# Optimization experiments

Measured on AMD Instinct MI355X. Metric: run time of the kernel, lower is better.

Reference implementation:

```python
import jax, jax.numpy as jnp
import numpy as np

L, U, D_IN, D_OUT, B = 6, 256, 784, 10, 32768  # num_layers, units, input_dim, output_dim, batch


def setup_inputs() -> dict:
    key = jax.random.key(0)
    ks = jax.random.split(key, 7)
    s = jnp.float32(0.05)  # keras 'random_normal' initializer stddev
    return {
        "x": jax.random.normal(ks[0], (B, D_IN), jnp.float32),
        "W_in": jax.random.normal(ks[1], (D_IN, U), jnp.float32) * s,
        "b_in": jax.random.normal(ks[2], (U,), jnp.float32) * s,
        "B0": jax.random.normal(ks[3], (L, U, U), jnp.float32) * s,   # per-layer B0
        "q": jax.random.normal(ks[4], (L, U), jnp.float32) * s,       # per-layer q
        "W_out": jax.random.normal(ks[5], (U, D_OUT), jnp.float32) * s,
        "b_out": jax.random.normal(ks[6], (D_OUT,), jnp.float32) * s,
    }


def reference(x, W_in, b_in, B0, q, W_out, b_out):
    u = W_in.shape[1]
    v0 = (x @ W_in + b_in).T          # (u, B)
    v1 = jnp.tanh(v0)                  # activation of layer 0 applied once before the loop

    def step(carry, params):
        v0, v1 = carry
        B0_l, q_l = params
        z = jnp.zeros((u, u), B0_l.dtype)
        # skew-symmetric block system [[0, B0], [-B0^T, 0]]
        A = jnp.block([[z, B0_l], [-B0_l.T, z]])           # (2u, 2u)
        rhs = jnp.concatenate([v0 + q_l[:, None], v1], 0)   # (2u, B)
        sol = jnp.linalg.solve(A, rhs)
        return (sol[:u], sol[u:]), None

    (v0, v1), _ = jax.lax.scan(step, (v0, v1), (B0, q))
    return v0.T @ W_out + b_out        # (B, D_OUT)
```

## Files before the change

kernel.cpp:

```cpp
#include <hip/hip_runtime.h>
#include <math.h>

#define NU      256
#define NLAYERS 6
#define NBATCH  32768
#define NDIN    784
#define NDOUT   10
#define NUSQ    65536

typedef unsigned short u16;
typedef __attribute__((ext_vector_type(8))) short s16x8;
typedef __attribute__((ext_vector_type(4))) float f32x4;

__device__ __forceinline__ u16 f2bf(float x) {
    union { float f; unsigned u; } a; a.f = x;
    const unsigned r = a.u + 0x7fffu + ((a.u >> 16) & 1u);
    return (u16)(r >> 16);
}
__device__ __forceinline__ float bf2f(u16 h) {
    union { unsigned u; float f; } a; a.u = ((unsigned)h) << 16; return a.f;
}

__device__ __forceinline__ void gl_lds16(const u16* g, u16* l) {
    __builtin_amdgcn_global_load_lds(
        (const __attribute__((address_space(1))) void*)g,
        (__attribute__((address_space(3))) void*)l, 16, 0, 0);
}

#define COL_CASES(BODY) \
    case 0:  BODY(0);  break; case 1:  BODY(1);  break; \
    case 2:  BODY(2);  break; case 3:  BODY(3);  break; \
    case 4:  BODY(4);  break; case 5:  BODY(5);  break; \
    case 6:  BODY(6);  break; case 7:  BODY(7);  break; \
    case 8:  BODY(8);  break; case 9:  BODY(9);  break; \
    case 10: BODY(10); break; case 11: BODY(11); break; \
    case 12: BODY(12); break; case 13: BODY(13); break; \
    case 14: BODY(14); break; case 15: BODY(15); break; \
    case 16: BODY(16); break; case 17: BODY(17); break; \
    case 18: BODY(18); break; case 19: BODY(19); break; \
    case 20: BODY(20); break; case 21: BODY(21); break; \
    case 22: BODY(22); break; case 23: BODY(23); break; \
    case 24: BODY(24); break; case 25: BODY(25); break; \
    case 26: BODY(26); break; case 27: BODY(27); break; \
    case 28: BODY(28); break; case 29: BODY(29); break; \
    case 30: BODY(30); break; case 31: BODY(31); break;

__global__ __launch_bounds__(512, 1) void fused_inv_ingemm(
    const float* __restrict__ B0, const float* __restrict__ qg,
    u16* __restrict__ wnnh, u16* __restrict__ wnnl,
    u16* __restrict__ wnth, u16* __restrict__ wntl,
    float* __restrict__ bq,
    const float* __restrict__ X, const float* __restrict__ Win,
    const float* __restrict__ bin,
    u16* __restrict__ V0h, u16* __restrict__ V0l,
    u16* __restrict__ V1h, u16* __restrict__ V1l)
{
    __shared__ __align__(16) float colv[2][256];
    __shared__ int   s_p[2];
    __shared__ float s_pv[2];
    __shared__ int   pivrow[256];
    __shared__ int   ilogrow[256];
    __shared__ float qs[256];
    __shared__ float part[8][256];
    __shared__ __align__(16) float As[16][128];
    __shared__ __align__(16) float Bs[16][128];

    const int tid = threadIdx.x;

    if (blockIdx.x < NLAYERS) {
        const int layer = blockIdx.x;
        const int ct = tid & 63;
        const int wv = tid >> 6;

        float a[32][4];
        const float* Ablk = B0 + (size_t)layer * NU * NU;
#pragma unroll
        for (int j = 0; j < 4; ++j) {
            const float* rp = Ablk + (size_t)(ct*4 + j)*NU + wv*32;
#pragma unroll
            for (int i = 0; i < 32; i += 4) {
                const float4 v = *(const float4*)(rp + i);
                a[i+0][j] = v.x; a[i+1][j] = v.y; a[i+2][j] = v.z; a[i+3][j] = v.w;
            }
        }

        int used = 0;

        for (int k = 0; k < 256; ++k) {
            const int wvk = k >> 5, ikk = k & 31, buf = k & 1;

            if (wv == wvk) {
                float c0, c1, c2, c3;
#define EXT(I) { c0 = a[I][0]; c1 = a[I][1]; c2 = a[I][2]; c3 = a[I][3]; }
                switch (ikk) { COL_CASES(EXT) }
#undef EXT
                float ba = -1.0f, bv = 1.0f; int br = 0;
                {
                    float av;
                    av = (used & 1) ? -1.0f : fabsf(c0);
                    if (av > ba) { ba = av; bv = c0; br = ct*4 + 0; }
                    av = (used & 2) ? -1.0f : fabsf(c1);
                    if (av > ba) { ba = av; bv = c1; br = ct*4 + 1; }
                    av = (used & 4) ? -1.0f : fabsf(c2);
                    if (av > ba) { ba = av; bv = c2; br = ct*4 + 2; }
                    av = (used & 8) ? -1.0f : fabsf(c3);
                    if (av > ba) { ba = av; bv = c3; br = ct*4 + 3; }
                }
#pragma unroll
                for (int off = 32; off > 0; off >>= 1) {
                    const float oa = __shfl_down(ba, off);
                    const float ov = __shfl_down(bv, off);
                    const int   orr = __shfl_down(br, off);
                    if (oa > ba) { ba = oa; bv = ov; br = orr; }
                }
                float4 cw; cw.x = c0; cw.y = c1; cw.z = c2; cw.w = c3;
                *(float4*)(&colv[buf][ct*4]) = cw;
                if (ct == 0) {
                    s_p[buf] = br;
                    s_pv[buf] = 1.0f / bv;
                    pivrow[k] = br;
                }
            }
            __syncthreads();

            const int   p      = __builtin_amdgcn_readfirstlane(s_p[buf]);
            const float pivinv = s_pv[buf];
            const int ctp = p >> 2, jp = p & 3;

            const float4 dv = *(const float4*)(&colv[buf][ct*4]);

            float t[32];
#define SEL(J) { _Pragma("unroll") for (int i = 0; i < 32; ++i) t[i] = a[i][J]; }
            switch (jp) {
                case 0: SEL(0) break; case 1: SEL(1) break;
                case 2: SEL(2) break; default: SEL(3) break;
            }
#undef SEL
            float prw[32];
#pragma unroll
            for (int i = 0; i < 32; ++i) prw[i] = __shfl(t[i], ctp) * pivinv;

            if (wv == wvk) {
#define ZCOL(I) { prw[I] = pivinv; a[I][0] = 0.0f; a[I][1] = 0.0f; a[I][2] = 0.0f; a[I][3] = 0.0f; }
                switch (ikk) { COL_CASES(ZCOL) }
#undef ZCOL
            }

            const float d0 = -dv.x, d1 = -dv.y, d2 = -dv.z, d3 = -dv.w;
#pragma unroll
            for (int i = 0; i < 32; ++i) {
                const float pw = prw[i];
                a[i][0] = fmaf(d0, pw, a[i][0]);
                a[i][1] = fmaf(d1, pw, a[i][1]);
                a[i][2] = fmaf(d2, pw, a[i][2]);
                a[i][3] = fmaf(d3, pw, a[i][3]);
            }

            const bool mine = (ct == ctp);
#define OWR(J) { _Pragma("unroll") for (int i = 0; i < 32; ++i) a[i][J] = mine ? prw[i] : a[i][J]; }
            switch (jp) {
                case 0: OWR(0) break; case 1: OWR(1) break;
                case 2: OWR(2) break; default: OWR(3) break;
            }
#undef OWR
            if (mine) used |= (1 << jp);
        }
        __syncthreads();

        if (tid < 256) { ilogrow[pivrow[tid]] = tid; qs[tid] = qg[(size_t)layer*NU + tid]; }
        __syncthreads();

        {
            float s0=0.f, s1=0.f, s2=0.f, s3=0.f;
#pragma unroll
            for (int i = 0; i < 32; ++i) {
                const float qq = qs[pivrow[wv*32 + i]];
                s0 = fmaf(a[i][0], qq, s0);
                s1 = fmaf(a[i][1], qq, s1);
                s2 = fmaf(a[i][2], qq, s2);
                s3 = fmaf(a[i][3], qq, s3);
            }
            part[wv][ct*4+0] = s0; part[wv][ct*4+1] = s1;
            part[wv][ct*4+2] = s2; part[wv][ct*4+3] = s3;
        }
        __syncthreads();
        if (tid < 256) {
            float s = 0.f;
#pragma unroll
            for (int w2 = 0; w2 < 8; ++w2) s += part[w2][tid];
            bq[(size_t)layer*NU + ilogrow[tid]] = s;
        }

        u16* nh = wnnh + (size_t)layer*NUSQ; u16* nl = wnnl + (size_t)layer*NUSQ;
        u16* th = wnth + (size_t)layer*NUSQ; u16* tl = wntl + (size_t)layer*NUSQ;
#pragma unroll
        for (int j = 0; j < 4; ++j) {
            const int r = ilogrow[ct*4 + j];
#pragma unroll
            for (int i = 0; i < 32; ++i) {
                const int c = pivrow[wv*32 + i];
                const float v = a[i][j];
                const u16 h  = f2bf(v);
                const u16 lo = f2bf(v - bf2f(h));
                th[(size_t)r*NU + c] = h;  tl[(size_t)r*NU + c] = lo;
                nh[(size_t)c*NU + r] = h;  nl[(size_t)c*NU + r] = lo;
            }
        }
        return;
    }

    if (tid >= 256) return;

    const int bid = blockIdx.x - NLAYERS;
    const int m0 = (bid & 255) * 128;
    const int n0 = (bid >> 8) * 128;
    const int t  = tid;
    const int tx = t & 15, ty = t >> 4;
    const int K = NDIN;

    float acc[8][8];
#pragma unroll
    for (int i = 0; i < 8; ++i)
#pragma unroll
        for (int j = 0; j < 8; ++j) acc[i][j] = 0.0f;

    const int am = t >> 1;
    const int ak = (t & 1) * 8;
    const int bk = t >> 4;
    const int bn = (t & 15) * 8;

    for (int k0 = 0; k0 < K; k0 += 16) {
        const float* Ap = X + (size_t)(m0 + am)*K + (k0 + ak);
        const float4 a0 = *(const float4*)(Ap);
        const float4 a1 = *(const float4*)(Ap + 4);
        As[ak+0][am] = a0.x; As[ak+1][am] = a0.y; As[ak+2][am] = a0.z; As[ak+3][am] = a0.w;
        As[ak+4][am] = a1.x; As[ak+5][am] = a1.y; As[ak+6][am] = a1.z; As[ak+7][am] = a1.w;
        const float* Bp = Win + (size_t)(k0 + bk)*NU + (n0 + bn);
        const float4 b0 = *(const float4*)(Bp);
        const float4 b1 = *(const float4*)(Bp + 4);
        *(float4*)(&Bs[bk][bn])   = b0;
        *(float4*)(&Bs[bk][bn+4]) = b1;
        __syncthreads();
#pragma unroll
        for (int kk = 0; kk < 16; ++kk) {
            float af[8], bf[8];
            *(float4*)(af)   = *(const float4*)(&As[kk][ty*8]);
            *(float4*)(af+4) = *(const float4*)(&As[kk][ty*8+4]);
            *(float4*)(bf)   = *(const float4*)(&Bs[kk][tx*8]);
            *(float4*)(bf+4) = *(const float4*)(&Bs[kk][tx*8+4]);
#pragma unroll
            for (int i = 0; i < 8; ++i)
#pragma unroll
                for (int j = 0; j < 8; ++j)
                    acc[i][j] = fmaf(af[i], bf[j], acc[i][j]);
        }
        __syncthreads();
    }

#pragma unroll
    for (int i = 0; i < 8; ++i) {
        const size_t row = m0 + ty*8 + i;
        s16x8 vh, vl, th2, tl2;
#pragma unroll
        for (int j = 0; j < 8; ++j) {
            const float v = acc[i][j] + bin[n0 + tx*8 + j];
            const u16 h  = f2bf(v);
            vh[j] = (short)h; vl[j] = (short)f2bf(v - bf2f(h));
            const float tv = tanhf(v);
            const u16 h2 = f2bf(tv);
            th2[j] = (short)h2; tl2[j] = (short)f2bf(tv - bf2f(h2));
        }
        const size_t o = row*NU + n0 + tx*8;
        *(s16x8*)&V0h[o] = vh; *(s16x8*)&V0l[o] = vl;
        *(s16x8*)&V1h[o] = th2; *(s16x8*)&V1l[o] = tl2;
    }
}

__global__ __launch_bounds__(256, 2) void gemm_mfma(
    const u16* __restrict__ Ah, const u16* __restrict__ Al,
    const u16* __restrict__ Bh, const u16* __restrict__ Bl,
    u16* __restrict__ Ch, u16* __restrict__ Cl,
    const float* __restrict__ bias, const float alpha)
{
    __shared__ __align__(16) u16 lAh[128*32], lAl[128*32], lBh[128*32], lBl[128*32];
    const int t    = threadIdx.x;
    const int lane = t & 63;
    const int w    = t >> 6;
    const int wr = w >> 1, wc = w & 1;
    const int qd = lane >> 4, l15 = lane & 15;
    const int m0 = blockIdx.x * 128, n0 = blockIdx.y * 128;

    const int srow = t >> 2;
    const int skc  = (t & 3) * 8;

    f32x4 acc[4][4];
    const f32x4 z = {0.f, 0.f, 0.f, 0.f};
#pragma unroll
    for (int i = 0; i < 4; ++i)
#pragma unroll
        for (int j = 0; j < 4; ++j) acc[i][j] = z;

    for (int k0 = 0; k0 < NU; k0 += 32) {
#pragma unroll
        for (int half = 0; half < 2; ++half) {
            const int rr = srow + half*64;
            const size_t ga = (size_t)(m0 + rr)*NU + k0 + skc;
            const size_t gb = (size_t)(n0 + rr)*NU + k0 + skc;
            const int lo = rr*32 + skc;
            gl_lds16(Ah + ga, &lAh[lo]);
            gl_lds16(Al + ga, &lAl[lo]);
            gl_lds16(Bh + gb, &lBh[lo]);
            gl_lds16(Bl + gb, &lBl[lo]);
        }
        __syncthreads();

        s16x8 ah[4], al[4], bh[4], bl[4];
#pragma unroll
        for (int mt = 0; mt < 4; ++mt) {
            const int off = (wr*64 + mt*16 + l15)*32 + qd*8;
            ah[mt] = *(const s16x8*)&lAh[off];
            al[mt] = *(const s16x8*)&lAl[off];
        }
#pragma unroll
        for (int nt = 0; nt < 4; ++nt) {
            const int off = (wc*64 + nt*16 + l15)*32 + qd*8;
            bh[nt] = *(const s16x8*)&lBh[off];
            bl[nt] = *(const s16x8*)&lBl[off];
        }
#pragma unroll
        for (int mt = 0; mt < 4; ++mt)
#pragma unroll
            for (int nt = 0; nt < 4; ++nt) {
                acc[mt][nt] = __builtin_amdgcn_mfma_f32_16x16x32_bf16(ah[mt], bh[nt], acc[mt][nt], 0, 0, 0);
                acc[mt][nt] = __builtin_amdgcn_mfma_f32_16x16x32_bf16(ah[mt], bl[nt], acc[mt][nt], 0, 0, 0);
                acc[mt][nt] = __builtin_amdgcn_mfma_f32_16x16x32_bf16(al[mt], bh[nt], acc[mt][nt], 0, 0, 0);
            }
        __syncthreads();
    }

#pragma unroll
    for (int mt = 0; mt < 4; ++mt) {
#pragma unroll
        for (int nt = 0; nt < 4; ++nt) {
            const int col = n0 + wc*64 + nt*16 + l15;
            const float bb = bias ? bias[col] : 0.0f;
#pragma unroll
            for (int r = 0; r < 4; ++r) {
                const int row = m0 + wr*64 + mt*16 + qd*4 + r;
                const float v = alpha*acc[mt][nt][r] + bb;
                const u16 h  = f2bf(v);
                const u16 lo = f2bf(v - bf2f(h));
                const size_t o = (size_t)row*NU + col;
                Ch[o] = h; Cl[o] = lo;
            }
        }
    }
}

__global__ __launch_bounds__(256) void out_gemm(
    const u16* __restrict__ V0h, const u16* __restrict__ V0l,
    const float* __restrict__ Wout,
    const float* __restrict__ bout, float* __restrict__ out)
{
    __shared__ float Ws[NU*NDOUT];
    const int t = threadIdx.x;
    for (int i = t; i < NU*NDOUT; i += 256) Ws[i] = Wout[i];
    __syncthreads();
    const int lane = t & 63;
    const int wv = t >> 6;
    const int row = blockIdx.x*4 + wv;
    float acc[NDOUT];
#pragma unroll
    for (int j = 0; j < NDOUT; ++j) acc[j] = 0.0f;
#pragma unroll
    for (int s = 0; s < 4; ++s) {
        const int k = lane + 64*s;
        const size_t o = (size_t)row*NU + k;
        const float v = bf2f(V0h[o]) + bf2f(V0l[o]);
#pragma unroll
        for (int j = 0; j < NDOUT; ++j) acc[j] = fmaf(v, Ws[k*NDOUT + j], acc[j]);
    }
#pragma unroll
    for (int off = 32; off > 0; off >>= 1) {
#pragma unroll
        for (int j = 0; j < NDOUT; ++j) acc[j] += __shfl_down(acc[j], off);
    }
    if (lane == 0) {
#pragma unroll
        for (int j = 0; j < NDOUT; ++j) out[(size_t)row*NDOUT + j] = acc[j] + bout[j];
    }
}

extern "C" void kernel_launch(void* const* d_in, const int* in_sizes, int n_in,
                              void* d_out, int out_size, void* d_ws, size_t ws_size,
                              hipStream_t stream)
{
    const float* x    = (const float*)d_in[0];
    const float* Win  = (const float*)d_in[1];
    const float* bin  = (const float*)d_in[2];
    const float* B0   = (const float*)d_in[3];
    const float* q    = (const float*)d_in[4];
    const float* Wout = (const float*)d_in[5];
    const float* bout = (const float*)d_in[6];
    float* out = (float*)d_out;

    u16* wnnh = (u16*)d_ws;
    u16* wnnl = wnnh + (size_t)NLAYERS*NUSQ;
    u16* wnth = wnnl + (size_t)NLAYERS*NUSQ;
    u16* wntl = wnth + (size_t)NLAYERS*NUSQ;
    float* bq = (float*)(wntl + (size_t)NLAYERS*NUSQ);
    u16* pl   = (u16*)(bq + NLAYERS*NU);
    const size_t PSZ = (size_t)NBATCH*NU;
    u16* sAh = pl;           u16* sAl = sAh + PSZ;
    u16* sBh = sAl + PSZ;    u16* sBl = sBh + PSZ;
    u16* sCh = sBl + PSZ;    u16* sCl = sCh + PSZ;

    fused_inv_ingemm<<<NLAYERS + 512, 512, 0, stream>>>(
        B0, q, wnnh, wnnl, wnth, wntl, bq,
        x, Win, bin, sAh, sAl, sBh, sBl);

    const dim3 ggrid(NBATCH/128, NU/128);

    u16 *v0h = sAh, *v0l = sAl, *v1h = sBh, *v1l = sBl, *frh = sCh, *frl = sCl;
    for (int l = 0; l < NLAYERS; ++l) {
        const size_t wo = (size_t)l*NUSQ;
        gemm_mfma<<<ggrid, 256, 0, stream>>>(v1h, v1l, wnnh + wo, wnnl + wo,
                                             frh, frl, nullptr, -1.0f);
        gemm_mfma<<<ggrid, 256, 0, stream>>>(v0h, v0l, wnth + wo, wntl + wo,
                                             v1h, v1l, bq + (size_t)l*NU, 1.0f);
        u16* t0 = v0h; u16* t1 = v0l;
        v0h = frh; v0l = frl; frh = t0; frl = t1;
    }
    out_gemm<<<NBATCH/4, 256, 0, stream>>>(v0h, v0l, Wout, bout, out);
}
```

Baseline: 1.021 ms.

## Widen fused inversion/input-GEMM kernel to 1024 threads with packed-key pivot search

Doubles the block size of the fused kernel so the per-layer Gauss-Jordan inversion spreads the 256 columns over 16 waves with 16 columns each, halving per-thread register state and serial FMA work per pivot step. The pivot search now packs |value| and row index into one unsigned key, reduced with a single xor-shuffle max, and reads the pivot value back with readlane. The input GEMM blocks now use 512 active threads with 8x4 micro-tiles. The packed key truncates the low mantissa bits, which can change pivot choice on near-ties, and the input-GEMM blocks now launch 1024 threads with half idle, which may reduce occupancy.

```diff
diff --git a/kernel.cpp b/kernel.cpp
--- a/kernel.cpp
+++ b/kernel.cpp
@@ -10,6 +10,7 @@
 
 typedef unsigned short u16;
 typedef __attribute__((ext_vector_type(8))) short s16x8;
+typedef __attribute__((ext_vector_type(4))) short s16x4;
 typedef __attribute__((ext_vector_type(4))) float f32x4;
 
 __device__ __forceinline__ u16 f2bf(float x) {
@@ -27,7 +28,24 @@
         (__attribute__((address_space(3))) void*)l, 16, 0, 0);
 }
 
-#define COL_CASES(BODY) \
+__device__ __forceinline__ float rlf(float v, int lane) {
+    return __int_as_float(__builtin_amdgcn_readlane(__float_as_int(v), lane));
+}
+
+__device__ __forceinline__ unsigned pkey(float v, int row) {
+    return (__float_as_uint(fabsf(v)) & 0xFFFFFF00u) | (unsigned)row;
+}
+
+__device__ __forceinline__ unsigned wave_umax64(unsigned key) {
+#pragma unroll
+    for (int off = 1; off < 64; off <<= 1) {
+        const unsigned o = (unsigned)__shfl_xor((int)key, off);
+        key = key > o ? key : o;
+    }
+    return key;
+}
+
+#define COL_CASES16(BODY) \
     case 0:  BODY(0);  break; case 1:  BODY(1);  break; \
     case 2:  BODY(2);  break; case 3:  BODY(3);  break; \
     case 4:  BODY(4);  break; case 5:  BODY(5);  break; \
@@ -35,17 +53,9 @@
     case 8:  BODY(8);  break; case 9:  BODY(9);  break; \
     case 10: BODY(10); break; case 11: BODY(11); break; \
     case 12: BODY(12); break; case 13: BODY(13); break; \
-    case 14: BODY(14); break; case 15: BODY(15); break; \
-    case 16: BODY(16); break; case 17: BODY(17); break; \
-    case 18: BODY(18); break; case 19: BODY(19); break; \
-    case 20: BODY(20); break; case 21: BODY(21); break; \
-    case 22: BODY(22); break; case 23: BODY(23); break; \
-    case 24: BODY(24); break; case 25: BODY(25); break; \
-    case 26: BODY(26); break; case 27: BODY(27); break; \
-    case 28: BODY(28); break; case 29: BODY(29); break; \
-    case 30: BODY(30); break; case 31: BODY(31); break;
-
-__global__ __launch_bounds__(512, 1) void fused_inv_ingemm(
+    case 14: BODY(14); break; case 15: BODY(15); break;
+
+__global__ __launch_bounds__(1024, 1) void fused_inv_ingemm(
     const float* __restrict__ B0, const float* __restrict__ qg,
     u16* __restrict__ wnnh, u16* __restrict__ wnnl,
     u16* __restrict__ wnth, u16* __restrict__ wntl,
@@ -61,7 +71,7 @@
     __shared__ int   pivrow[256];
     __shared__ int   ilogrow[256];
     __shared__ float qs[256];
-    __shared__ float part[8][256];
+    __shared__ float part[16][256];
     __shared__ __align__(16) float As[16][128];
     __shared__ __align__(16) float Bs[16][128];
 
@@ -72,13 +82,13 @@
         const int ct = tid & 63;
         const int wv = tid >> 6;
 
-        float a[32][4];
+        float a[16][4];
         const float* Ablk = B0 + (size_t)layer * NU * NU;
 #pragma unroll
         for (int j = 0; j < 4; ++j) {
-            const float* rp = Ablk + (size_t)(ct*4 + j)*NU + wv*32;
-#pragma unroll
-            for (int i = 0; i < 32; i += 4) {
+            const float* rp = Ablk + (size_t)(ct*4 + j)*NU + wv*16;
+#pragma unroll
+            for (int i = 0; i < 16; i += 4) {
                 const float4 v = *(const float4*)(rp + i);
                 a[i+0][j] = v.x; a[i+1][j] = v.y; a[i+2][j] = v.z; a[i+3][j] = v.w;
             }
@@ -87,38 +97,32 @@
         int used = 0;
 
         for (int k = 0; k < 256; ++k) {
-            const int wvk = k >> 5, ikk = k & 31, buf = k & 1;
+            const int wvk = k >> 4, ikk = k & 15, buf = k & 1;
 
             if (wv == wvk) {
                 float c0, c1, c2, c3;
 #define EXT(I) { c0 = a[I][0]; c1 = a[I][1]; c2 = a[I][2]; c3 = a[I][3]; }
-                switch (ikk) { COL_CASES(EXT) }
+                switch (ikk) { COL_CASES16(EXT) }
 #undef EXT
-                float ba = -1.0f, bv = 1.0f; int br = 0;
-                {
-                    float av;
-                    av = (used & 1) ? -1.0f : fabsf(c0);
-                    if (av > ba) { ba = av; bv = c0; br = ct*4 + 0; }
-                    av = (used & 2) ? -1.0f : fabsf(c1);
-                    if (av > ba) { ba = av; bv = c1; br = ct*4 + 1; }
-                    av = (used & 4) ? -1.0f : fabsf(c2);
-                    if (av > ba) { ba = av; bv = c2; br = ct*4 + 2; }
-                    av = (used & 8) ? -1.0f : fabsf(c3);
-                    if (av > ba) { ba = av; bv = c3; br = ct*4 + 3; }
-                }
-#pragma unroll
-                for (int off = 32; off > 0; off >>= 1) {
-                    const float oa = __shfl_down(ba, off);
-                    const float ov = __shfl_down(bv, off);
-                    const int   orr = __shfl_down(br, off);
-                    if (oa > ba) { ba = oa; bv = ov; br = orr; }
+                unsigned key = (used & 1) ? 0u : pkey(c0, ct*4 + 0);
+                unsigned q1  = (used & 2) ? 0u : pkey(c1, ct*4 + 1); key = key > q1 ? key : q1;
+                unsigned q2  = (used & 4) ? 0u : pkey(c2, ct*4 + 2); key = key > q2 ? key : q2;
+                unsigned q3  = (used & 8) ? 0u : pkey(c3, ct*4 + 3); key = key > q3 ? key : q3;
+                key = wave_umax64(key);
+                const int pn = __builtin_amdgcn_readfirstlane((int)(key & 255u));
+                float bv;
+                switch (pn & 3) {
+                    case 0: bv = rlf(c0, pn >> 2); break;
+                    case 1: bv = rlf(c1, pn >> 2); break;
+                    case 2: bv = rlf(c2, pn >> 2); break;
+                    default: bv = rlf(c3, pn >> 2); break;
                 }
                 float4 cw; cw.x = c0; cw.y = c1; cw.z = c2; cw.w = c3;
                 *(float4*)(&colv[buf][ct*4]) = cw;
                 if (ct == 0) {
-                    s_p[buf] = br;
+                    s_p[buf] = pn;
                     s_pv[buf] = 1.0f / bv;
-                    pivrow[k] = br;
+                    pivrow[k] = pn;
                 }
             }
             __syncthreads();
@@ -129,26 +133,26 @@
 
             const float4 dv = *(const float4*)(&colv[buf][ct*4]);
 
-            float t[32];
-#define SEL(J) { _Pragma("unroll") for (int i = 0; i < 32; ++i) t[i] = a[i][J]; }
+            float t[16];
+#define SEL(J) { _Pragma("unroll") for (int i = 0; i < 16; ++i) t[i] = a[i][J]; }
             switch (jp) {
                 case 0: SEL(0) break; case 1: SEL(1) break;
                 case 2: SEL(2) break; default: SEL(3) break;
             }
 #undef SEL
-            float prw[32];
-#pragma unroll
-            for (int i = 0; i < 32; ++i) prw[i] = __shfl(t[i], ctp) * pivinv;
+            float prw[16];
+#pragma unroll
+            for (int i = 0; i < 16; ++i) prw[i] = __shfl(t[i], ctp) * pivinv;
 
             if (wv == wvk) {
 #define ZCOL(I) { prw[I] = pivinv; a[I][0] = 0.0f; a[I][1] = 0.0f; a[I][2] = 0.0f; a[I][3] = 0.0f; }
-                switch (ikk) { COL_CASES(ZCOL) }
+                switch (ikk) { COL_CASES16(ZCOL) }
 #undef ZCOL
             }
 
             const float d0 = -dv.x, d1 = -dv.y, d2 = -dv.z, d3 = -dv.w;
 #pragma unroll
-            for (int i = 0; i < 32; ++i) {
+            for (int i = 0; i < 16; ++i) {
                 const float pw = prw[i];
                 a[i][0] = fmaf(d0, pw, a[i][0]);
                 a[i][1] = fmaf(d1, pw, a[i][1]);
@@ -157,7 +161,7 @@
             }
 
             const bool mine = (ct == ctp);
-#define OWR(J) { _Pragma("unroll") for (int i = 0; i < 32; ++i) a[i][J] = mine ? prw[i] : a[i][J]; }
+#define OWR(J) { _Pragma("unroll") for (int i = 0; i < 16; ++i) a[i][J] = mine ? prw[i] : a[i][J]; }
             switch (jp) {
                 case 0: OWR(0) break; case 1: OWR(1) break;
                 case 2: OWR(2) break; default: OWR(3) break;
@@ -173,8 +177,8 @@
         {
             float s0=0.f, s1=0.f, s2=0.f, s3=0.f;
 #pragma unroll
-            for (int i = 0; i < 32; ++i) {
-                const float qq = qs[pivrow[wv*32 + i]];
+            for (int i = 0; i < 16; ++i) {
+                const float qq = qs[pivrow[wv*16 + i]];
                 s0 = fmaf(a[i][0], qq, s0);
                 s1 = fmaf(a[i][1], qq, s1);
                 s2 = fmaf(a[i][2], qq, s2);
@@ -187,7 +191,7 @@
         if (tid < 256) {
             float s = 0.f;
 #pragma unroll
-            for (int w2 = 0; w2 < 8; ++w2) s += part[w2][tid];
+            for (int w2 = 0; w2 < 16; ++w2) s += part[w2][tid];
             bq[(size_t)layer*NU + ilogrow[tid]] = s;
         }
 
@@ -197,8 +201,8 @@
         for (int j = 0; j < 4; ++j) {
             const int r = ilogrow[ct*4 + j];
 #pragma unroll
-            for (int i = 0; i < 32; ++i) {
-                const int c = pivrow[wv*32 + i];
+            for (int i = 0; i < 16; ++i) {
+                const int c = pivrow[wv*16 + i];
                 const float v = a[i][j];
                 const u16 h  = f2bf(v);
                 const u16 lo = f2bf(v - bf2f(h));
@@ -209,49 +213,42 @@
         return;
     }
 
-    if (tid >= 256) return;
+    if (tid >= 512) return;
 
     const int bid = blockIdx.x - NLAYERS;
     const int m0 = (bid & 255) * 128;
     const int n0 = (bid >> 8) * 128;
     const int t  = tid;
-    const int tx = t & 15, ty = t >> 4;
+    const int tx = t & 31, ty = t >> 5;
     const int K = NDIN;
 
-    float acc[8][8];
+    float acc[8][4];
 #pragma unroll
     for (int i = 0; i < 8; ++i)
 #pragma unroll
-        for (int j = 0; j < 8; ++j) acc[i][j] = 0.0f;
-
-    const int am = t >> 1;
-    const int ak = (t & 1) * 8;
-    const int bk = t >> 4;
-    const int bn = (t & 15) * 8;
+        for (int j = 0; j < 4; ++j) acc[i][j] = 0.0f;
+
+    const int am = t >> 2;
+    const int ak = (t & 3) * 4;
+    const int bk = t >> 5;
+    const int bn = (t & 31) * 4;
 
     for (int k0 = 0; k0 < K; k0 += 16) {
-        const float* Ap = X + (size_t)(m0 + am)*K + (k0 + ak);
-        const float4 a0 = *(const float4*)(Ap);
-        const float4 a1 = *(const float4*)(Ap + 4);
+        const float4 a0 = *(const float4*)(X + (size_t)(m0 + am)*K + (k0 + ak));
         As[ak+0][am] = a0.x; As[ak+1][am] = a0.y; As[ak+2][am] = a0.z; As[ak+3][am] = a0.w;
-        As[ak+4][am] = a1.x; As[ak+5][am] = a1.y; As[ak+6][am] = a1.z; As[ak+7][am] = a1.w;
-        const float* Bp = Win + (size_t)(k0 + bk)*NU + (n0 + bn);
-        const float4 b0 = *(const float4*)(Bp);
-        const float4 b1 = *(const float4*)(Bp + 4);
-        *(float4*)(&Bs[bk][bn])   = b0;
-        *(float4*)(&Bs[bk][bn+4]) = b1;
+        const float4 b0 = *(const float4*)(Win + (size_t)(k0 + bk)*NU + (n0 + bn));
+        *(float4*)(&Bs[bk][bn]) = b0;
         __syncthreads();
 #pragma unroll
         for (int kk = 0; kk < 16; ++kk) {
-            float af[8], bf[8];
+            float af[8], bf[4];
             *(float4*)(af)   = *(const float4*)(&As[kk][ty*8]);
             *(float4*)(af+4) = *(const float4*)(&As[kk][ty*8+4]);
-            *(float4*)(bf)   = *(const float4*)(&Bs[kk][tx*8]);
-            *(float4*)(bf+4) = *(const float4*)(&Bs[kk][tx*8+4]);
+            *(float4*)(bf)   = *(const float4*)(&Bs[kk][tx*4]);
 #pragma unroll
             for (int i = 0; i < 8; ++i)
 #pragma unroll
-                for (int j = 0; j < 8; ++j)
+                for (int j = 0; j < 4; ++j)
                     acc[i][j] = fmaf(af[i], bf[j], acc[i][j]);
         }
         __syncthreads();
@@ -260,19 +257,19 @@
 #pragma unroll
     for (int i = 0; i < 8; ++i) {
         const size_t row = m0 + ty*8 + i;
-        s16x8 vh, vl, th2, tl2;
-#pragma unroll
-        for (int j = 0; j < 8; ++j) {
-            const float v = acc[i][j] + bin[n0 + tx*8 + j];
+        s16x4 vh, vl, th2, tl2;
+#pragma unroll
+        for (int j = 0; j < 4; ++j) {
+            const float v = acc[i][j] + bin[n0 + tx*4 + j];
             const u16 h  = f2bf(v);
             vh[j] = (short)h; vl[j] = (short)f2bf(v - bf2f(h));
             const float tv = tanhf(v);
             const u16 h2 = f2bf(tv);
             th2[j] = (short)h2; tl2[j] = (short)f2bf(tv - bf2f(h2));
         }
-        const size_t o = row*NU + n0 + tx*8;
-        *(s16x8*)&V0h[o] = vh; *(s16x8*)&V0l[o] = vl;
-        *(s16x8*)&V1h[o] = th2; *(s16x8*)&V1l[o] = tl2;
+        const size_t o = row*NU + n0 + tx*4;
+        *(s16x4*)&V0h[o] = vh; *(s16x4*)&V0l[o] = vl;
+        *(s16x4*)&V1h[o] = th2; *(s16x4*)&V1l[o] = tl2;
     }
 }
 
@@ -415,7 +412,7 @@
     u16* sBh = sAl + PSZ;    u16* sBl = sBh + PSZ;
     u16* sCh = sBl + PSZ;    u16* sCl = sCh + PSZ;
 
-    fused_inv_ingemm<<<NLAYERS + 512, 512, 0, stream>>>(
+    fused_inv_ingemm<<<NLAYERS + 512, 1024, 0, stream>>>(
         B0, q, wnnh, wnnl, wnth, wntl, bq,
         x, Win, bin, sAh, sAl, sBh, sBl);
 
```

Result: slower. 1.832 ms (+79.4%).
